# Optimization experiments

Measured on AMD Instinct MI355X. Metric: run time of the kernel, lower is better.

The kernel has to match this reference:

```python
import jax, jax.numpy as jnp
import numpy as np

N_NODES = 100000
N_EDGES = 640000
IN_CH, HID_CH, OUT_CH = 256, 128, 64


def setup_inputs() -> dict:
    key = jax.random.key(0)
    ks = jax.random.split(key, 6)
    x = jax.random.normal(ks[0], (N_NODES, IN_CH), dtype=jnp.float32)
    edge_index = jax.random.randint(ks[1], (2, N_EDGES), 0, N_NODES, dtype=jnp.int32)
    # Glorot-style init for GCNConv weights
    W1 = jax.random.normal(ks[2], (IN_CH, HID_CH), dtype=jnp.float32) * (1.0 / np.sqrt(IN_CH))
    W_mu = jax.random.normal(ks[3], (HID_CH, OUT_CH), dtype=jnp.float32) * (1.0 / np.sqrt(HID_CH))
    W_logvar = jax.random.normal(ks[4], (HID_CH, OUT_CH), dtype=jnp.float32) * (1.0 / np.sqrt(HID_CH))
    return {
        "x": x,
        "edge_index": edge_index,
        "W1": W1,
        "b1": jnp.zeros((HID_CH,), jnp.float32),
        "W_mu": W_mu,
        "b_mu": jnp.zeros((OUT_CH,), jnp.float32),
        "W_logvar": W_logvar,
        "b_logvar": jnp.zeros((OUT_CH,), jnp.float32),
    }


def reference(x, edge_index, W1, b1, W_mu, b_mu, W_logvar, b_logvar):
    N = x.shape[0]
    # PyG GCNConv default: add self-loops, symmetric normalization D^-1/2 A_hat D^-1/2
    loops = jnp.arange(N, dtype=edge_index.dtype)
    src = jnp.concatenate([edge_index[0], loops])  # [E+N]
    dst = jnp.concatenate([edge_index[1], loops])  # [E+N]
    deg = jax.ops.segment_sum(jnp.ones_like(src, dtype=x.dtype), dst, num_segments=N)
    dinv = jax.lax.rsqrt(deg)  # deg >= 1 due to self-loops
    norm = dinv[src] * dinv[dst]  # [E+N]

    def gcn_conv(h, W, b):
        h = h @ W                                   # [N, d_out]
        msg = h[src] * norm[:, None]                # gather + scale  [E+N, d_out]
        out = jax.ops.segment_sum(msg, dst, num_segments=N)  # scatter-add
        return out + b

    h = jax.nn.relu(gcn_conv(x, W1, b1))
    mu = gcn_conv(h, W_mu, b_mu)
    logvar = gcn_conv(h, W_logvar, b_logvar)
    return (mu, logvar)
```

## Files before the change

kernel.cpp:

```cpp
#include <hip/hip_runtime.h>
#include <hip/hip_bf16.h>

#define N_NODES 100000
#define E_EDGES 640000

typedef __attribute__((ext_vector_type(8))) short short8;
typedef __attribute__((ext_vector_type(4))) float float4v;

__device__ __forceinline__ float bf2f(unsigned int u16) {
    union { unsigned int i; float f; } c; c.i = u16 << 16; return c.f;
}
__device__ __forceinline__ unsigned short f2bf(float f) {
    union { float f; unsigned int i; } c; c.f = f;
    unsigned int x = c.i;
    unsigned int r = (x + 0x7fffu + ((x >> 16) & 1u)) >> 16;
    return (unsigned short)r;
}

#define ASYNC16NT(g, l)                                                        \
    __builtin_amdgcn_global_load_lds(                                          \
        (const __attribute__((address_space(1))) void*)(g),                    \
        (__attribute__((address_space(3))) void*)(l), 16, 0, 2)

#define WS_HIST    0
#define WS_CURSOR  524288
#define WS_OFFS    1048576
#define WS_DINV    1572864
#define WS_BSUMS   2097152
#define WS_EIDX    2621440
#define WS_WP1     7864320
#define WS_WP2     7929856
#define WS_H0      7962624
#define WS_H       33562624

#define NB_E 2500
__global__ __launch_bounds__(256) void k_hist_pack(const int* __restrict__ dst, int* __restrict__ hist,
                                                   const float* __restrict__ W1,
                                                   const float* __restrict__ Wmu,
                                                   const float* __restrict__ Wlv,
                                                   unsigned short* __restrict__ Wp1,
                                                   unsigned short* __restrict__ Wp2) {
    int b = blockIdx.x;
    if (b < NB_E) {
        int e = b * 256 + threadIdx.x;
        if (e < E_EDGES) atomicAdd(&hist[__builtin_nontemporal_load(dst + e)], 1);
    } else {
        int i = (b - NB_E) * 256 + threadIdx.x;
        if (i < 256 * 128) {
            int k = i >> 7, n = i & 127;
            Wp1[n * 256 + k] = f2bf(W1[i]);
        }
        if (i < 128 * 128) {
            int k = i >> 7, n = i & 127;
            float w = (n < 64) ? Wmu[k * 64 + n] : Wlv[k * 64 + (n - 64)];
            Wp2[n * 128 + k] = f2bf(w);
        }
    }
}

__global__ __launch_bounds__(256) void k_scan1(const int* __restrict__ hist,
                                               int* __restrict__ offs,
                                               int* __restrict__ bsums,
                                               float* __restrict__ dinv) {
    __shared__ int sd[256];
    int t = threadIdx.x;
    int base = blockIdx.x * 1024 + t * 4;
    int v[4];
#pragma unroll
    for (int j = 0; j < 4; ++j) v[j] = (base + j < N_NODES) ? hist[base + j] : 0;
#pragma unroll
    for (int j = 0; j < 4; ++j)
        if (base + j < N_NODES) dinv[base + j] = rsqrtf((float)(v[j] + 1));
    int s = v[0] + v[1] + v[2] + v[3];
    sd[t] = s;
    __syncthreads();
    for (int d = 1; d < 256; d <<= 1) {
        int x = (t >= d) ? sd[t - d] : 0;
        __syncthreads();
        sd[t] += x;
        __syncthreads();
    }
    int excl = sd[t] - s;
    if (t == 255) bsums[blockIdx.x] = sd[255];
    int run = excl;
#pragma unroll
    for (int j = 0; j < 4; ++j) {
        if (base + j < N_NODES) offs[base + j] = run;
        run += v[j];
    }
}

__global__ __launch_bounds__(128) void k_scan2(int* __restrict__ bsums, int nb) {
    __shared__ int sd[128];
    int t = threadIdx.x;
    int v = (t < nb) ? bsums[t] : 0;
    sd[t] = v;
    __syncthreads();
    for (int d = 1; d < 128; d <<= 1) {
        int x = (t >= d) ? sd[t - d] : 0;
        __syncthreads();
        sd[t] += x;
        __syncthreads();
    }
    if (t < nb) bsums[t] = sd[t] - v;
}

__global__ __launch_bounds__(256) void k_fill(const int* __restrict__ src, const int* __restrict__ dst,
                                              const int* __restrict__ offs, const int* __restrict__ bsums,
                                              int* __restrict__ cursor,
                                              const float* __restrict__ dinv,
                                              int2* __restrict__ eidx) {
    int e = blockIdx.x * 256 + threadIdx.x;
    if (e < E_EDGES) {
        int s = __builtin_nontemporal_load(src + e);
        int d = __builtin_nontemporal_load(dst + e);
        int p = offs[d] + bsums[d >> 10] + atomicAdd(&cursor[d], 1);
        int2 v;
        v.x = s;
        v.y = __float_as_int(dinv[s] * dinv[d]);
        eidx[p] = v;
    }
}

__global__ __launch_bounds__(256, 6) void k_mgemm1(const float* __restrict__ A,
                                                   const unsigned short* __restrict__ Bpack,
                                                   unsigned short* __restrict__ out) {
    __shared__ float As[64 * 32];
    __shared__ unsigned short Bs[128 * 40];
    int tid = threadIdx.x;
    int row0 = blockIdx.x * 64;
    int wave = tid >> 6, lane = tid & 63;
    int c = lane & 15, q = lane >> 4;
    int wrow = (wave >> 1) * 32, wcol = (wave & 1) * 64;

    float4v acc[2][4];
#pragma unroll
    for (int i = 0; i < 2; ++i)
#pragma unroll
        for (int j = 0; j < 4; ++j) acc[i][j] = (float4v){0.f, 0.f, 0.f, 0.f};

    int srow = tid >> 1;
    int shalf = (tid & 1) * 16;

    for (int k0 = 0; k0 < 256; k0 += 32) {
        const unsigned short* bsrc = Bpack + (size_t)srow * 256 + k0 + shalf;
        short8 b0 = *(const short8*)(bsrc);
        short8 b1 = *(const short8*)(bsrc + 8);
#pragma unroll
        for (int t = 0; t < 2; ++t) {
            int grp = t * 4 + wave;
            int S = grp * 64 + lane;
            int row = S >> 3, j = S & 7;
            int kq = j ^ (row & 7);
            const float* g = A + (size_t)(row0 + row) * 256 + k0 + kq * 4;
            float* ldst = As + grp * 256;
            if (row0 + row < N_NODES) ASYNC16NT(g, ldst);
        }
        *(short8*)(&Bs[srow * 40 + shalf])     = b0;
        *(short8*)(&Bs[srow * 40 + shalf + 8]) = b1;
        __syncthreads();

        short8 af[2], bfr[4];
#pragma unroll
        for (int mt = 0; mt < 2; ++mt) {
            int r = wrow + mt * 16 + c;
            int j0 = (q * 2) ^ (r & 7);
            float4v fa = *(const float4v*)(&As[r * 32 + j0 * 4]);
            float4v fb = *(const float4v*)(&As[r * 32 + (j0 ^ 1) * 4]);
            short8 s;
#pragma unroll
            for (int jj = 0; jj < 4; ++jj) s[jj]     = (short)f2bf(fa[jj]);
#pragma unroll
            for (int jj = 0; jj < 4; ++jj) s[4 + jj] = (short)f2bf(fb[jj]);
            af[mt] = s;
        }
#pragma unroll
        for (int nt = 0; nt < 4; ++nt)
            bfr[nt] = *(const short8*)(&Bs[(wcol + nt * 16 + c) * 40 + q * 8]);
#pragma unroll
        for (int mt = 0; mt < 2; ++mt)
#pragma unroll
            for (int nt = 0; nt < 4; ++nt)
                acc[mt][nt] = __builtin_amdgcn_mfma_f32_16x16x32_bf16(af[mt], bfr[nt], acc[mt][nt], 0, 0, 0);
        __syncthreads();
    }

#pragma unroll
    for (int mt = 0; mt < 2; ++mt) {
#pragma unroll
        for (int i = 0; i < 4; ++i) {
            int row = row0 + wrow + mt * 16 + q * 4 + i;
            if (row >= N_NODES) continue;
#pragma unroll
            for (int nt = 0; nt < 4; ++nt) {
                int cc = wcol + nt * 16 + c;
                out[(size_t)row * 128 + cc] = f2bf(acc[mt][nt][i]);
            }
        }
    }
}

__global__ __launch_bounds__(256, 6) void k_mgemm2(const unsigned short* __restrict__ A,
                                                   const unsigned short* __restrict__ Bpack,
                                                   const float* __restrict__ bias0,
                                                   const float* __restrict__ bias1,
                                                   float* __restrict__ out) {
    constexpr int LDT = 40;
    __shared__ unsigned short As[64 * LDT];
    __shared__ unsigned short Bs[128 * LDT];
    int tid = threadIdx.x;
    int row0 = blockIdx.x * 64;
    int wave = tid >> 6, lane = tid & 63;
    int c = lane & 15, q = lane >> 4;
    int wrow = (wave >> 1) * 32, wcol = (wave & 1) * 64;

    float4v acc[2][4];
#pragma unroll
    for (int i = 0; i < 2; ++i)
#pragma unroll
        for (int j = 0; j < 4; ++j) acc[i][j] = (float4v){0.f, 0.f, 0.f, 0.f};

    int srow = tid >> 1, shalf = (tid & 1) * 16;
    int arow = tid >> 2, aoff = (tid & 3) * 8;
    const short8 zed = {0, 0, 0, 0, 0, 0, 0, 0};

    for (int k0 = 0; k0 < 128; k0 += 32) {
        const unsigned short* bsrc = Bpack + (size_t)srow * 128 + k0 + shalf;
        short8 b0 = *(const short8*)(bsrc);
        short8 b1 = *(const short8*)(bsrc + 8);
        int grow = row0 + arow;
        short8 a0 = zed;
        if (grow < N_NODES)
            a0 = *(const short8*)(A + (size_t)grow * 128 + k0 + aoff);
        *(short8*)(&Bs[srow * LDT + shalf])     = b0;
        *(short8*)(&Bs[srow * LDT + shalf + 8]) = b1;
        *(short8*)(&As[arow * LDT + aoff])      = a0;
        __syncthreads();

        short8 af[2], bfr[4];
#pragma unroll
        for (int mt = 0; mt < 2; ++mt)
            af[mt] = *(const short8*)(&As[(wrow + mt * 16 + c) * LDT + q * 8]);
#pragma unroll
        for (int nt = 0; nt < 4; ++nt)
            bfr[nt] = *(const short8*)(&Bs[(wcol + nt * 16 + c) * LDT + q * 8]);
#pragma unroll
        for (int mt = 0; mt < 2; ++mt)
#pragma unroll
            for (int nt = 0; nt < 4; ++nt)
                acc[mt][nt] = __builtin_amdgcn_mfma_f32_16x16x32_bf16(af[mt], bfr[nt], acc[mt][nt], 0, 0, 0);
        __syncthreads();
    }

#pragma unroll
    for (int mt = 0; mt < 2; ++mt) {
#pragma unroll
        for (int i = 0; i < 4; ++i) {
            int row = row0 + wrow + mt * 16 + q * 4 + i;
            if (row >= N_NODES) continue;
#pragma unroll
            for (int nt = 0; nt < 4; ++nt) {
                int cc = wcol + nt * 16 + c;
                float v = acc[mt][nt][i];
                if (cc < 64) out[(size_t)row * 64 + cc] = v + bias0[cc];
                else out[(size_t)N_NODES * 64 + (size_t)row * 64 + (cc - 64)] = v + bias1[cc - 64];
            }
        }
    }
}

template <int BIAS_RELU>
__global__ __launch_bounds__(256) void k_agg(const unsigned int* __restrict__ in,
                                             unsigned int* __restrict__ out,
                                             const float* __restrict__ dinv,
                                             const int2* __restrict__ eidx,
                                             const int* __restrict__ offs,
                                             const int* __restrict__ bsums,
                                             const int* __restrict__ cnt,
                                             const float* __restrict__ bias) {
    int wid = (blockIdx.x * 256 + threadIdx.x) >> 6;
    if (wid >= N_NODES) return;
    int l = threadIdx.x & 63;
    float di = dinv[wid];
    unsigned int u = in[(size_t)wid * 64 + l];
    float sc = di * di;
    float ax = sc * bf2f(u & 0xffffu);
    float ay = sc * bf2f(u >> 16);
    if (BIAS_RELU) { ax += bias[2 * l]; ay += bias[2 * l + 1]; }
    int start = offs[wid] + bsums[wid >> 10];
    int n = cnt[wid];

    for (int base = 0; base < n; base += 64) {
        int m = min(n - base, 64);
        int sreg = 0; float wreg = 0.f;
        if (l < m) {
            int2 ev = eidx[start + base + l];
            sreg = ev.x;
            wreg = __int_as_float(ev.y);
        }
        int e = 0;
        for (; e + 4 <= m; e += 4) {
            int s0 = __shfl(sreg, e),     s1 = __shfl(sreg, e + 1);
            int s2 = __shfl(sreg, e + 2), s3 = __shfl(sreg, e + 3);
            float w0 = __shfl(wreg, e),     w1 = __shfl(wreg, e + 1);
            float w2 = __shfl(wreg, e + 2), w3 = __shfl(wreg, e + 3);
            unsigned int u0 = in[(size_t)s0 * 64 + l];
            unsigned int u1 = in[(size_t)s1 * 64 + l];
            unsigned int u2 = in[(size_t)s2 * 64 + l];
            unsigned int u3 = in[(size_t)s3 * 64 + l];
            ax += w0 * bf2f(u0 & 0xffffu); ay += w0 * bf2f(u0 >> 16);
            ax += w1 * bf2f(u1 & 0xffffu); ay += w1 * bf2f(u1 >> 16);
            ax += w2 * bf2f(u2 & 0xffffu); ay += w2 * bf2f(u2 >> 16);
            ax += w3 * bf2f(u3 & 0xffffu); ay += w3 * bf2f(u3 >> 16);
        }
        for (; e < m; ++e) {
            int s0 = __shfl(sreg, e);
            float w0 = __shfl(wreg, e);
            unsigned int u0 = in[(size_t)s0 * 64 + l];
            ax += w0 * bf2f(u0 & 0xffffu); ay += w0 * bf2f(u0 >> 16);
        }
    }
    if (BIAS_RELU) { ax = fmaxf(ax, 0.f); ay = fmaxf(ay, 0.f); }
    out[(size_t)wid * 64 + l] = (unsigned int)f2bf(ax) | ((unsigned int)f2bf(ay) << 16);
}

extern "C" void kernel_launch(void* const* d_in, const int* in_sizes, int n_in,
                              void* d_out, int out_size, void* d_ws, size_t ws_size,
                              hipStream_t stream) {
    const float* x    = (const float*)d_in[0];
    const int*   ei   = (const int*)d_in[1];
    const float* W1   = (const float*)d_in[2];
    const float* b1   = (const float*)d_in[3];
    const float* Wmu  = (const float*)d_in[4];
    const float* bmu  = (const float*)d_in[5];
    const float* Wlv  = (const float*)d_in[6];
    const float* blv  = (const float*)d_in[7];
    float* outp = (float*)d_out;

    const int* src = ei;
    const int* dst = ei + E_EDGES;

    char* ws = (char*)d_ws;
    int*            hist   = (int*)(ws + WS_HIST);
    int*            cursor = (int*)(ws + WS_CURSOR);
    int*            offs   = (int*)(ws + WS_OFFS);
    float*          dinv   = (float*)(ws + WS_DINV);
    int*            bsums  = (int*)(ws + WS_BSUMS);
    int2*           eidx   = (int2*)(ws + WS_EIDX);
    unsigned short* Wp1    = (unsigned short*)(ws + WS_WP1);
    unsigned short* Wp2    = (unsigned short*)(ws + WS_WP2);
    unsigned short* h0     = (unsigned short*)(ws + WS_H0);
    unsigned short* h      = (unsigned short*)(ws + WS_H);

    const int NB_S = (N_NODES + 1023) / 1024;
    const int NB_G = (N_NODES + 63) / 64;

    hipMemsetAsync(ws + WS_HIST, 0, 1048576, stream);
    k_hist_pack<<<NB_E + 128, 256, 0, stream>>>(dst, hist, W1, Wmu, Wlv, Wp1, Wp2);
    k_scan1<<<NB_S, 256, 0, stream>>>(hist, offs, bsums, dinv);
    k_scan2<<<1, 128, 0, stream>>>(bsums, NB_S);
    k_fill<<<NB_E, 256, 0, stream>>>(src, dst, offs, bsums, cursor, dinv, eidx);

    k_mgemm1<<<NB_G, 256, 0, stream>>>(x, Wp1, h0);
    k_agg<1><<<(N_NODES * 64 + 255) / 256, 256, 0, stream>>>(
        (const unsigned int*)h0, (unsigned int*)h, dinv, eidx, offs, bsums, hist, b1);

    k_agg<0><<<(N_NODES * 64 + 255) / 256, 256, 0, stream>>>(
        (const unsigned int*)h, (unsigned int*)h0, dinv, eidx, offs, bsums, hist, nullptr);
    k_mgemm2<<<NB_G, 256, 0, stream>>>(h0, Wp2, bmu, blv, outp);
}
```

Before: 345.6 us.

## Fuse second-layer aggregation with the mu/logvar GEMM through shared memory

Merges the second sparse aggregation and the output GEMM into one kernel. Each 512-thread block first aggregates 64 nodes (8 rows per wave) into an LDS tile in bf16, then runs the MFMA GEMM against the packed mu/logvar weights straight from LDS. This drops the global write and re-read of the aggregated hidden matrix, plus one kernel launch. In exchange each wave processes rows serially, and the large LDS footprint may limit occupancy during the latency-bound gather phase.

```diff
diff --git a/kernel.cpp b/kernel.cpp
--- a/kernel.cpp
+++ b/kernel.cpp
@@ -200,93 +200,22 @@
     }
 }
 
-__global__ __launch_bounds__(256, 6) void k_mgemm2(const unsigned short* __restrict__ A,
-                                                   const unsigned short* __restrict__ Bpack,
-                                                   const float* __restrict__ bias0,
-                                                   const float* __restrict__ bias1,
-                                                   float* __restrict__ out) {
-    constexpr int LDT = 40;
-    __shared__ unsigned short As[64 * LDT];
-    __shared__ unsigned short Bs[128 * LDT];
-    int tid = threadIdx.x;
-    int row0 = blockIdx.x * 64;
-    int wave = tid >> 6, lane = tid & 63;
-    int c = lane & 15, q = lane >> 4;
-    int wrow = (wave >> 1) * 32, wcol = (wave & 1) * 64;
-
-    float4v acc[2][4];
-#pragma unroll
-    for (int i = 0; i < 2; ++i)
-#pragma unroll
-        for (int j = 0; j < 4; ++j) acc[i][j] = (float4v){0.f, 0.f, 0.f, 0.f};
-
-    int srow = tid >> 1, shalf = (tid & 1) * 16;
-    int arow = tid >> 2, aoff = (tid & 3) * 8;
-    const short8 zed = {0, 0, 0, 0, 0, 0, 0, 0};
-
-    for (int k0 = 0; k0 < 128; k0 += 32) {
-        const unsigned short* bsrc = Bpack + (size_t)srow * 128 + k0 + shalf;
-        short8 b0 = *(const short8*)(bsrc);
-        short8 b1 = *(const short8*)(bsrc + 8);
-        int grow = row0 + arow;
-        short8 a0 = zed;
-        if (grow < N_NODES)
-            a0 = *(const short8*)(A + (size_t)grow * 128 + k0 + aoff);
-        *(short8*)(&Bs[srow * LDT + shalf])     = b0;
-        *(short8*)(&Bs[srow * LDT + shalf + 8]) = b1;
-        *(short8*)(&As[arow * LDT + aoff])      = a0;
-        __syncthreads();
-
-        short8 af[2], bfr[4];
-#pragma unroll
-        for (int mt = 0; mt < 2; ++mt)
-            af[mt] = *(const short8*)(&As[(wrow + mt * 16 + c) * LDT + q * 8]);
-#pragma unroll
-        for (int nt = 0; nt < 4; ++nt)
-            bfr[nt] = *(const short8*)(&Bs[(wcol + nt * 16 + c) * LDT + q * 8]);
-#pragma unroll
-        for (int mt = 0; mt < 2; ++mt)
-#pragma unroll
-            for (int nt = 0; nt < 4; ++nt)
-                acc[mt][nt] = __builtin_amdgcn_mfma_f32_16x16x32_bf16(af[mt], bfr[nt], acc[mt][nt], 0, 0, 0);
-        __syncthreads();
-    }
-
-#pragma unroll
-    for (int mt = 0; mt < 2; ++mt) {
-#pragma unroll
-        for (int i = 0; i < 4; ++i) {
-            int row = row0 + wrow + mt * 16 + q * 4 + i;
-            if (row >= N_NODES) continue;
-#pragma unroll
-            for (int nt = 0; nt < 4; ++nt) {
-                int cc = wcol + nt * 16 + c;
-                float v = acc[mt][nt][i];
-                if (cc < 64) out[(size_t)row * 64 + cc] = v + bias0[cc];
-                else out[(size_t)N_NODES * 64 + (size_t)row * 64 + (cc - 64)] = v + bias1[cc - 64];
-            }
-        }
-    }
-}
-
-template <int BIAS_RELU>
-__global__ __launch_bounds__(256) void k_agg(const unsigned int* __restrict__ in,
-                                             unsigned int* __restrict__ out,
-                                             const float* __restrict__ dinv,
-                                             const int2* __restrict__ eidx,
-                                             const int* __restrict__ offs,
-                                             const int* __restrict__ bsums,
-                                             const int* __restrict__ cnt,
-                                             const float* __restrict__ bias) {
+__global__ __launch_bounds__(256) void k_agg1(const unsigned int* __restrict__ in,
+                                              unsigned int* __restrict__ out,
+                                              const float* __restrict__ dinv,
+                                              const int2* __restrict__ eidx,
+                                              const int* __restrict__ offs,
+                                              const int* __restrict__ bsums,
+                                              const int* __restrict__ cnt,
+                                              const float* __restrict__ bias) {
     int wid = (blockIdx.x * 256 + threadIdx.x) >> 6;
     if (wid >= N_NODES) return;
     int l = threadIdx.x & 63;
     float di = dinv[wid];
     unsigned int u = in[(size_t)wid * 64 + l];
     float sc = di * di;
-    float ax = sc * bf2f(u & 0xffffu);
-    float ay = sc * bf2f(u >> 16);
-    if (BIAS_RELU) { ax += bias[2 * l]; ay += bias[2 * l + 1]; }
+    float ax = sc * bf2f(u & 0xffffu) + bias[2 * l];
+    float ay = sc * bf2f(u >> 16) + bias[2 * l + 1];
     int start = offs[wid] + bsums[wid >> 10];
     int n = cnt[wid];
 
@@ -320,8 +249,125 @@
             ax += w0 * bf2f(u0 & 0xffffu); ay += w0 * bf2f(u0 >> 16);
         }
     }
-    if (BIAS_RELU) { ax = fmaxf(ax, 0.f); ay = fmaxf(ay, 0.f); }
+    ax = fmaxf(ax, 0.f); ay = fmaxf(ay, 0.f);
     out[(size_t)wid * 64 + l] = (unsigned int)f2bf(ax) | ((unsigned int)f2bf(ay) << 16);
+}
+
+__global__ __launch_bounds__(512, 8) void k_agg2mm(const unsigned int* __restrict__ in,
+                                                   const float* __restrict__ dinv,
+                                                   const int2* __restrict__ eidx,
+                                                   const int* __restrict__ offs,
+                                                   const int* __restrict__ bsums,
+                                                   const int* __restrict__ cnt,
+                                                   const unsigned short* __restrict__ Bpack,
+                                                   const float* __restrict__ bias0,
+                                                   const float* __restrict__ bias1,
+                                                   float* __restrict__ out) {
+    __shared__ unsigned short As4[4 * 64 * 40];
+    __shared__ unsigned short Bs[128 * 40];
+    int tid = threadIdx.x;
+    int row0 = blockIdx.x * 64;
+    int wave = tid >> 6, lane = tid & 63;
+    int l = lane;
+
+    unsigned int* As4w = (unsigned int*)As4;
+    int ui = (l >> 4) * 1280 + (l & 15);
+#pragma unroll 1
+    for (int i = 0; i < 8; ++i) {
+        int lr = wave * 8 + i;
+        int nd = row0 + lr;
+        float ax = 0.f, ay = 0.f;
+        if (nd < N_NODES) {
+            float di = dinv[nd];
+            unsigned int u = in[(size_t)nd * 64 + l];
+            float sc = di * di;
+            ax = sc * bf2f(u & 0xffffu);
+            ay = sc * bf2f(u >> 16);
+            int start = offs[nd] + bsums[nd >> 10];
+            int n = cnt[nd];
+            for (int base = 0; base < n; base += 64) {
+                int m = min(n - base, 64);
+                int sreg = 0; float wreg = 0.f;
+                if (l < m) {
+                    int2 ev = eidx[start + base + l];
+                    sreg = ev.x;
+                    wreg = __int_as_float(ev.y);
+                }
+                int e = 0;
+                for (; e + 4 <= m; e += 4) {
+                    int s0 = __shfl(sreg, e),     s1 = __shfl(sreg, e + 1);
+                    int s2 = __shfl(sreg, e + 2), s3 = __shfl(sreg, e + 3);
+                    float w0 = __shfl(wreg, e),     w1 = __shfl(wreg, e + 1);
+                    float w2 = __shfl(wreg, e + 2), w3 = __shfl(wreg, e + 3);
+                    unsigned int u0 = in[(size_t)s0 * 64 + l];
+                    unsigned int u1 = in[(size_t)s1 * 64 + l];
+                    unsigned int u2 = in[(size_t)s2 * 64 + l];
+                    unsigned int u3 = in[(size_t)s3 * 64 + l];
+                    ax += w0 * bf2f(u0 & 0xffffu); ay += w0 * bf2f(u0 >> 16);
+                    ax += w1 * bf2f(u1 & 0xffffu); ay += w1 * bf2f(u1 >> 16);
+                    ax += w2 * bf2f(u2 & 0xffffu); ay += w2 * bf2f(u2 >> 16);
+                    ax += w3 * bf2f(u3 & 0xffffu); ay += w3 * bf2f(u3 >> 16);
+                }
+                for (; e < m; ++e) {
+                    int s0 = __shfl(sreg, e);
+                    float w0 = __shfl(wreg, e);
+                    unsigned int u0 = in[(size_t)s0 * 64 + l];
+                    ax += w0 * bf2f(u0 & 0xffffu); ay += w0 * bf2f(u0 >> 16);
+                }
+            }
+        }
+        As4w[ui + lr * 20] = (unsigned int)f2bf(ax) | ((unsigned int)f2bf(ay) << 16);
+    }
+
+    int c = lane & 15, q = lane >> 4;
+    int wm = wave >> 2, wn = wave & 3;
+    int wrow = wm * 32, wcol = wn * 32;
+
+    float4v acc[2][2];
+#pragma unroll
+    for (int i = 0; i < 2; ++i)
+#pragma unroll
+        for (int j = 0; j < 2; ++j) acc[i][j] = (float4v){0.f, 0.f, 0.f, 0.f};
+
+    int srow = tid >> 2;
+    int soff = (tid & 3) * 8;
+
+    for (int kc = 0; kc < 4; ++kc) {
+        int k0 = kc * 32;
+        short8 b0 = *(const short8*)(Bpack + (size_t)srow * 128 + k0 + soff);
+        __syncthreads();
+        *(short8*)(&Bs[srow * 40 + soff]) = b0;
+        __syncthreads();
+
+        short8 af[2], bfr[2];
+#pragma unroll
+        for (int mt = 0; mt < 2; ++mt)
+            af[mt] = *(const short8*)(&As4[kc * 2560 + (wrow + mt * 16 + c) * 40 + q * 8]);
+#pragma unroll
+        for (int nt = 0; nt < 2; ++nt)
+            bfr[nt] = *(const short8*)(&Bs[(wcol + nt * 16 + c) * 40 + q * 8]);
+#pragma unroll
+        for (int mt = 0; mt < 2; ++mt)
+#pragma unroll
+            for (int nt = 0; nt < 2; ++nt)
+                acc[mt][nt] = __builtin_amdgcn_mfma_f32_16x16x32_bf16(af[mt], bfr[nt], acc[mt][nt], 0, 0, 0);
+    }
+
+#pragma unroll
+    for (int mt = 0; mt < 2; ++mt) {
+#pragma unroll
+        for (int i = 0; i < 4; ++i) {
+            int row = row0 + wrow + mt * 16 + q * 4 + i;
+            if (row >= N_NODES) continue;
+#pragma unroll
+            for (int nt = 0; nt < 2; ++nt) {
+                int cc = wcol + nt * 16 + c;
+                float v = acc[mt][nt][i];
+                if (cc < 64) out[(size_t)row * 64 + cc] = v + bias0[cc];
+                else out[(size_t)N_NODES * 64 + (size_t)row * 64 + (cc - 64)] = v + bias1[cc - 64];
+            }
+        }
+    }
 }
 
 extern "C" void kernel_launch(void* const* d_in, const int* in_sizes, int n_in,
@@ -362,10 +408,9 @@
     k_fill<<<NB_E, 256, 0, stream>>>(src, dst, offs, bsums, cursor, dinv, eidx);
 
     k_mgemm1<<<NB_G, 256, 0, stream>>>(x, Wp1, h0);
-    k_agg<1><<<(N_NODES * 64 + 255) / 256, 256, 0, stream>>>(
+    k_agg1<<<(N_NODES * 64 + 255) / 256, 256, 0, stream>>>(
         (const unsigned int*)h0, (unsigned int*)h, dinv, eidx, offs, bsums, hist, b1);
 
-    k_agg<0><<<(N_NODES * 64 + 255) / 256, 256, 0, stream>>>(
-        (const unsigned int*)h, (unsigned int*)h0, dinv, eidx, offs, bsums, hist, nullptr);
-    k_mgemm2<<<NB_G, 256, 0, stream>>>(h0, Wp2, bmu, blv, outp);
-}
+    k_agg2mm<<<NB_G, 512, 0, stream>>>(
+        (const unsigned int*)h, dinv, eidx, offs, bsums, hist, Wp2, bmu, blv, outp);
+}
```

After: 339.1 us. No clear change (-1.9%).
